# Optimization experiments

Measured on AMD Instinct MI355X. Metric: run time of the kernel, lower is better.

The kernel has to match this reference:

```python
import jax, jax.numpy as jnp
import numpy as np

B, N, T, L, H = 8, 128, 256, 32, 128


def setup_inputs() -> dict:
    key = jax.random.key(0)
    k0, k1, k2, k3, k4, k5 = jax.random.split(key, 6)
    x = jax.random.uniform(k0, (B, N, T), dtype=jnp.float32)
    s = 1.0 / np.sqrt(H)  # pytorch LSTM/Linear default init scale
    W_ih = jax.random.uniform(k1, (N, 4 * H, L), minval=-s, maxval=s, dtype=jnp.float32)
    b_ih = jax.random.uniform(k2, (N, 4 * H), minval=-s, maxval=s, dtype=jnp.float32)
    b_hh = jax.random.uniform(k3, (N, 4 * H), minval=-s, maxval=s, dtype=jnp.float32)
    W_fc = jax.random.uniform(k4, (N, N, H), minval=-s, maxval=s, dtype=jnp.float32)  # [node_i, out_j, H]
    b_fc = jax.random.uniform(k5, (N, N), minval=-s, maxval=s, dtype=jnp.float32)  # [node_i, out_j]
    return {"x": x, "W_ih": W_ih, "b_ih": b_ih, "b_hh": b_hh, "W_fc": W_fc, "b_fc": b_fc}


def reference(x, W_ih, b_ih, b_hh, W_fc, b_fc):
    # x: [B, N, T]
    Bn, Nn, Tn = x.shape
    Ln = W_ih.shape[-1]
    Hh = W_fc.shape[-1]
    Ttau = Tn - Ln  # number of prediction steps (t = L .. T-1)

    # Sliding windows x[:, i, tau:tau+L] for tau = 0..Ttau-1  -> [B, N, Ttau, L]
    idx = jnp.arange(Ttau)[:, None] + jnp.arange(Ln)[None, :]  # [Ttau, L]
    xw = x[:, :, idx]

    # Single-step LSTM with zero initial state: W_hh term vanishes.
    gates = jnp.einsum('bntl,ngl->bntg', xw, W_ih) + (b_ih + b_hh)[None, :, None, :]
    gi, gf, gg, go = jnp.split(gates, 4, axis=-1)  # pytorch order: i, f, g, o
    c = jax.nn.sigmoid(gi) * jnp.tanh(gg)          # f*c0 = 0
    h = jax.nn.sigmoid(go) * jnp.tanh(c)           # [B, N, Ttau, H]

    # Per-node fc (grouped GEMM): contributions[b, tau, j, i]
    contrib = jnp.einsum('bnth,njh->btjn', h, W_fc) + b_fc.T[None, None, :, :]

    # G[b, j, i] = mean_tau contrib[b, tau, j, i] / x[b, i, L + tau]
    denom = jnp.transpose(x[:, :, Ln:], (0, 2, 1))[:, :, None, :]  # [B, Ttau, 1, N_i]
    G = jnp.mean(contrib / denom, axis=1)                          # [B, N, N]

    X_hat = jnp.sum(contrib, axis=2) + 1e-6  # [B, Ttau, N]
    return G, X_hat
```

## Files before the change

### kernel.cpp

```cpp
#include <hip/hip_runtime.h>
#include <math.h>

#define B_  8
#define N_  128
#define T_  256
#define L_  32
#define H_  128
#define TT_ 224

typedef float f2    __attribute__((ext_vector_type(2)));
typedef float f4    __attribute__((ext_vector_type(4)));
typedef float f32x4 __attribute__((ext_vector_type(4)));
typedef short bf16x8 __attribute__((ext_vector_type(8)));

#define L2E_  1.4426950408889634f
#define L2E2_ 2.8853900817779268f

__device__ __forceinline__ unsigned pk2bf(float a, float b) {
    unsigned ua = __float_as_uint(a), ub = __float_as_uint(b);
    ua = (ua + 0x7FFFu + ((ua >> 16) & 1u)) >> 16;
    ub = (ub + 0x7FFFu + ((ub >> 16) & 1u)) >> 16;
    return ua | (ub << 16);
}
__device__ __forceinline__ float aexp2(float x) {
    float r; asm("v_exp_f32 %0, %1" : "=v"(r) : "v"(x)); return r;
}
__device__ __forceinline__ float aexp2n(float x) {
    float r; asm("v_exp_f32 %0, -%1" : "=v"(r) : "v"(x)); return r;
}
__device__ __forceinline__ float arcp(float x) {
    return __builtin_amdgcn_rcpf(x);
}

__global__ __launch_bounds__(256)
void k_pre(const float* __restrict__ W_ih, const float* __restrict__ W_fc,
           const float* __restrict__ b_ih, const float* __restrict__ b_hh,
           const float* __restrict__ b_fc,
           unsigned short* __restrict__ W3sw, float* __restrict__ wsum,
           float* __restrict__ bsum, float* __restrict__ bia_g) {
    const int n   = blockIdx.x;
    const int pid = blockIdx.y;
    const int tid = threadIdx.x;
    if (pid < 6) {
        const int idx  = pid * 256 + tid;
        const int fg   = idx >> 6;
        const int lane = idx & 63;
        const int col  = lane & 15, quad = lane >> 4;
        const int g    = fg % 3, ht = fg / 3;
        const int r    = g * 128 + ht * 16 + col;
        const int sr   = r + (r >= 128 ? 128 : 0);
        const float sc = (g == 1) ? L2E2_ : L2E_;
        const f4* src = (const f4*)(W_ih + (size_t)n * 512 * L_ + sr * L_ + quad * 8);
        f4 v0 = src[0] * sc, v1 = src[1] * sc;
        uint4 out;
        out.x = pk2bf(v0.x, v0.y); out.y = pk2bf(v0.z, v0.w);
        out.z = pk2bf(v1.x, v1.y); out.w = pk2bf(v1.z, v1.w);
        *(uint4*)&W3sw[((size_t)n * 1536 + idx) * 8] = out;
    } else {
        __shared__ f4 part[8][32];
        __shared__ float bp[2];
        {
            const int h4 = tid & 31, jg = tid >> 5;
            const f4* Wf = (const f4*)(W_fc + (size_t)n * N_ * H_) + (size_t)jg * 16 * 32 + h4;
            f4 s = {0.f, 0.f, 0.f, 0.f};
            #pragma unroll
            for (int j = 0; j < 16; ++j) s += Wf[j * 32];
            part[jg][h4] = s;
        }
        if (tid < 128) {
            float bv = b_fc[n * N_ + tid];
            #pragma unroll
            for (int off = 32; off > 0; off >>= 1) bv += __shfl_down(bv, off, 64);
            if ((tid & 63) == 0) bp[tid >> 6] = bv;
        }
        for (int i = tid; i < 384; i += 256) {
            const int sr = i + (i >= 128 ? 128 : 0);
            const float sc = (i >= 128 && i < 256) ? L2E2_ : L2E_;
            bia_g[n * 384 + i] =
                (b_ih[(size_t)n * 512 + sr] + b_hh[(size_t)n * 512 + sr]) * sc;
        }
        __syncthreads();
        if (tid < 32) {
            f4 s = part[0][tid];
            #pragma unroll
            for (int jg = 1; jg < 8; ++jg) s += part[jg][tid];
            *(f4*)&wsum[n * H_ + tid * 4] = s;
        }
        if (tid == 0) bsum[n] = bp[0] + bp[1];
    }
}

__global__ __launch_bounds__(256)
__attribute__((amdgpu_waves_per_eu(4, 4)))
void k_main(const float* __restrict__ x,
            const unsigned short* __restrict__ W3sw,
            const float* __restrict__ bia_g,
            const float* __restrict__ wsum, const float* __restrict__ bsum,
            const float* __restrict__ W_fc, const float* __restrict__ b_fc,
            float* __restrict__ G, float* __restrict__ xhat) {
    const int n   = blockIdx.x;
    const int b   = blockIdx.y;
    const int tid = threadIdx.x;
    const int w    = tid >> 6;
    const int lane = tid & 63;
    const int col  = lane & 15;
    const int quad = lane >> 4;

    __shared__ float xs[258];
    __shared__ unsigned xeo[2][128];
    __shared__ float xr[TT_];
    __shared__ uint4 xA[14 * 64];
    __shared__ float xh_part[4][TT_];
    __shared__ float hd_loc[H_];
    __shared__ float red[4];

    const uint4* wsw = (const uint4*)W3sw + (size_t)n * 24 * 64 + lane;
    union { uint4 u; bf16x8 v; } bfr[2][3];
    float biaL[2][3], wshL[2];
    #pragma unroll
    for (int ht2 = 0; ht2 < 2; ++ht2) {
        const int ht = 2 * w + ht2;
        #pragma unroll
        for (int g = 0; g < 3; ++g) {
            bfr[ht2][g].u = wsw[(size_t)(ht * 3 + g) * 64];
            biaL[ht2][g]  = bia_g[n * 384 + g * 128 + ht * 16 + col];
        }
        wshL[ht2] = wsum[n * H_ + ht * 16 + col];
    }
    const float bsum_n = bsum[n];

    xs[tid] = x[((size_t)b * N_ + n) * T_ + tid];
    if (tid < 2) xs[256 + tid] = 0.f;
    __syncthreads();
    if (tid < TT_) xr[tid] = 1.0f / xs[L_ + tid];
    if (tid < 128) {
        xeo[0][tid] = pk2bf(xs[2 * tid],     xs[2 * tid + 1]);
        xeo[1][tid] = pk2bf(xs[2 * tid + 1], xs[2 * tid + 2]);
    }
    __syncthreads();
    for (int e = tid; e < 14 * 64; e += 256) {
        const int tt = e >> 6, ln = e & 63;
        const int s  = tt * 16 + (ln & 15) + (ln >> 4) * 8;
        const int p  = s & 1, base = s >> 1;
        uint4 v;
        v.x = xeo[p][base + 0]; v.y = xeo[p][base + 1];
        v.z = xeo[p][base + 2]; v.w = xeo[p][base + 3];
        xA[e] = v;
    }
    __syncthreads();

    float hd_acc[2] = {0.f, 0.f};
    const f32x4 zero4 = {0.f, 0.f, 0.f, 0.f};

    #pragma unroll 2
    for (int ttile = 0; ttile < 14; ++ttile) {
        union { uint4 u; bf16x8 v; } af;
        af.u = xA[ttile * 64 + lane];

        const f4 xr4 = *(const f4*)&xr[ttile * 16 + quad * 4];
        float px[4];

        #pragma unroll
        for (int ht2 = 0; ht2 < 2; ++ht2) {
            f32x4 ai = __builtin_amdgcn_mfma_f32_16x16x32_bf16(af.v, bfr[ht2][0].v, zero4, 0, 0, 0);
            f32x4 ag = __builtin_amdgcn_mfma_f32_16x16x32_bf16(af.v, bfr[ht2][1].v, zero4, 0, 0, 0);
            f32x4 ao = __builtin_amdgcn_mfma_f32_16x16x32_bf16(af.v, bfr[ht2][2].v, zero4, 0, 0, 0);
            #pragma unroll
            for (int pr = 0; pr < 2; ++pr) {
                f2 gi = {ai[2*pr] + biaL[ht2][0], ai[2*pr+1] + biaL[ht2][0]};
                f2 gg = {ag[2*pr] + biaL[ht2][1], ag[2*pr+1] + biaL[ht2][1]};
                f2 go = {ao[2*pr] + biaL[ht2][2], ao[2*pr+1] + biaL[ht2][2]};
                f2 e1 = {aexp2n(gi.x), aexp2n(gi.y)};
                f2 e2 = {aexp2(gg.x),  aexp2(gg.y)};
                f2 e3 = {aexp2n(go.x), aexp2n(go.y)};
                const f2 A  = (1.f + e1) * (e2 + 1.f);
                const f2 Bv = 1.f + e3;
                const f2 AB = A * Bv;
                f2 R  = {arcp(AB.x), arcp(AB.y)};
                const f2 em = e2 - 1.f;
                const f2 t  = em * R;
                const f2 c  = t * Bv;
                const f2 c2 = c * c;
                f2 Q = c2 * -0.027698f + 0.120833f;
                Q = c2 * Q - 0.331541f;
                Q = c2 * Q + 1.0f;
                const f2 hh = t * (Q * c);
                const f2 hhv = t * Q;
                hd_acc[ht2] = fmaf(hhv.x, xr4[2*pr],   hd_acc[ht2]);
                hd_acc[ht2] = fmaf(hhv.y, xr4[2*pr+1], hd_acc[ht2]);
                px[2*pr]   = hhv.x * wshL[ht2] + (ht2 ? px[2*pr]   : 0.f);
                px[2*pr+1] = hhv.y * wshL[ht2] + (ht2 ? px[2*pr+1] : 0.f);
                (void)hh;
            }
        }
        #pragma unroll
        for (int reg = 0; reg < 4; ++reg) {
            float pv = px[reg];
            pv += __shfl_xor(pv, 1, 64);
            pv += __shfl_xor(pv, 2, 64);
            pv += __shfl_xor(pv, 4, 64);
            pv += __shfl_xor(pv, 8, 64);
            if (col == 0) xh_part[w][ttile * 16 + quad * 4 + reg] = pv;
        }
    }

    #pragma unroll
    for (int ht2 = 0; ht2 < 2; ++ht2) {
        float v = hd_acc[ht2];
        v += __shfl_xor(v, 16, 64);
        v += __shfl_xor(v, 32, 64);
        if (lane < 16) hd_loc[(2 * w + ht2) * 16 + lane] = v;
    }
    {
        float dv = (tid < TT_) ? xr[tid] : 0.f;
        #pragma unroll
        for (int off = 32; off > 0; off >>= 1) dv += __shfl_down(dv, off, 64);
        if (lane == 0) red[w] = dv;
    }
    __syncthreads();

    if (tid < TT_) {
        const float v = xh_part[0][tid] + xh_part[1][tid] +
                        xh_part[2][tid] + xh_part[3][tid];
        xhat[((size_t)b * TT_ + tid) * N_ + n] = v + bsum_n + 1e-6f;
    }

    {
        const float dinv = red[0] + red[1] + red[2] + red[3];
        const int j    = tid >> 1;
        const int half = tid & 1;
        const f4* Wf = (const f4*)(W_fc + ((size_t)n * N_ + j) * H_ + half * 64);
        float s = 0.f;
        #pragma unroll
        for (int q = 0; q < 16; ++q) {
            const f4 wv = Wf[q];
            const int hb = half * 64 + q * 4;
            s = fmaf(wv.x, hd_loc[hb + 0],
                fmaf(wv.y, hd_loc[hb + 1],
                fmaf(wv.z, hd_loc[hb + 2],
                fmaf(wv.w, hd_loc[hb + 3], s))));
        }
        s += __shfl_xor(s, 1, 64);
        if (half == 0) {
            const float bj = b_fc[n * N_ + j];
            G[(size_t)b * N_ * N_ + (size_t)j * N_ + n] =
                (s + bj * dinv) * (1.0f / 224.0f);
        }
    }
}

extern "C" void kernel_launch(void* const* d_in, const int* in_sizes, int n_in,
                              void* d_out, int out_size, void* d_ws, size_t ws_size,
                              hipStream_t stream) {
    const float* x    = (const float*)d_in[0];
    const float* W_ih = (const float*)d_in[1];
    const float* b_ih = (const float*)d_in[2];
    const float* b_hh = (const float*)d_in[3];
    const float* W_fc = (const float*)d_in[4];
    const float* b_fc = (const float*)d_in[5];

    float* G    = (float*)d_out;
    float* xhat = (float*)d_out + (size_t)B_ * N_ * N_;

    unsigned short* W3sw = (unsigned short*)d_ws;
    float* wsum   = (float*)(W3sw + (size_t)N_ * 1536 * 8);
    float* bsum   = wsum + N_ * H_;
    float* bia_g  = bsum + N_;

    k_pre<<<dim3(N_, 7), dim3(256), 0, stream>>>(W_ih, W_fc, b_ih, b_hh, b_fc,
                                                 W3sw, wsum, bsum, bia_g);
    k_main<<<dim3(N_, B_), dim3(256), 0, stream>>>(x, W3sw, bia_g, wsum, bsum,
                                                   W_fc, b_fc, G, xhat);
}
```

Before: 110.9 us.

## Split time tiles across two wave groups with 512-thread blocks in k_main

Doubles the k_main block to 512 threads. Waves are split into four hidden-tile groups and two time groups, so each wave handles 7 time tiles instead of 14. The per-time-group hidden partial sums go into a second shared buffer and are added during the W_fc dot product, which now uses four threads per output row. This cuts the serial MFMA and transcendental loop per wave to raise parallelism, at the cost of more threads per block and possible register pressure under the relaxed waves-per-EU bound.

```diff
diff --git a/kernel.cpp b/kernel.cpp
--- a/kernel.cpp
+++ b/kernel.cpp
@@ -90,18 +90,20 @@
     }
 }
 
-__global__ __launch_bounds__(256)
-__attribute__((amdgpu_waves_per_eu(4, 4)))
+__global__ __launch_bounds__(512)
+__attribute__((amdgpu_waves_per_eu(4, 8)))
 void k_main(const float* __restrict__ x,
             const unsigned short* __restrict__ W3sw,
             const float* __restrict__ bia_g,
             const float* __restrict__ wsum, const float* __restrict__ bsum,
             const float* __restrict__ W_fc, const float* __restrict__ b_fc,
             float* __restrict__ G, float* __restrict__ xhat) {
-    const int n   = blockIdx.x;
-    const int b   = blockIdx.y;
-    const int tid = threadIdx.x;
+    const int n    = blockIdx.x;
+    const int b    = blockIdx.y;
+    const int tid  = threadIdx.x;
     const int w    = tid >> 6;
+    const int hgrp = w & 3;
+    const int tgrp = w >> 2;
     const int lane = tid & 63;
     const int col  = lane & 15;
     const int quad = lane >> 4;
@@ -111,7 +113,7 @@
     __shared__ float xr[TT_];
     __shared__ uint4 xA[14 * 64];
     __shared__ float xh_part[4][TT_];
-    __shared__ float hd_loc[H_];
+    __shared__ float hd_loc2[2][H_];
     __shared__ float red[4];
 
     const uint4* wsw = (const uint4*)W3sw + (size_t)n * 24 * 64 + lane;
@@ -119,7 +121,7 @@
     float biaL[2][3], wshL[2];
     #pragma unroll
     for (int ht2 = 0; ht2 < 2; ++ht2) {
-        const int ht = 2 * w + ht2;
+        const int ht = 2 * hgrp + ht2;
         #pragma unroll
         for (int g = 0; g < 3; ++g) {
             bfr[ht2][g].u = wsw[(size_t)(ht * 3 + g) * 64];
@@ -129,8 +131,8 @@
     }
     const float bsum_n = bsum[n];
 
-    xs[tid] = x[((size_t)b * N_ + n) * T_ + tid];
-    if (tid < 2) xs[256 + tid] = 0.f;
+    if (tid < 256) xs[tid] = x[((size_t)b * N_ + n) * T_ + tid];
+    if (tid >= 256 && tid < 258) xs[tid] = 0.f;
     __syncthreads();
     if (tid < TT_) xr[tid] = 1.0f / xs[L_ + tid];
     if (tid < 128) {
@@ -138,7 +140,7 @@
         xeo[1][tid] = pk2bf(xs[2 * tid + 1], xs[2 * tid + 2]);
     }
     __syncthreads();
-    for (int e = tid; e < 14 * 64; e += 256) {
+    for (int e = tid; e < 14 * 64; e += 512) {
         const int tt = e >> 6, ln = e & 63;
         const int s  = tt * 16 + (ln & 15) + (ln >> 4) * 8;
         const int p  = s & 1, base = s >> 1;
@@ -153,7 +155,8 @@
     const f32x4 zero4 = {0.f, 0.f, 0.f, 0.f};
 
     #pragma unroll 2
-    for (int ttile = 0; ttile < 14; ++ttile) {
+    for (int tt2 = 0; tt2 < 7; ++tt2) {
+        const int ttile = tgrp * 7 + tt2;
         union { uint4 u; bf16x8 v; } af;
         af.u = xA[ttile * 64 + lane];
 
@@ -184,13 +187,11 @@
                 f2 Q = c2 * -0.027698f + 0.120833f;
                 Q = c2 * Q - 0.331541f;
                 Q = c2 * Q + 1.0f;
-                const f2 hh = t * (Q * c);
                 const f2 hhv = t * Q;
                 hd_acc[ht2] = fmaf(hhv.x, xr4[2*pr],   hd_acc[ht2]);
                 hd_acc[ht2] = fmaf(hhv.y, xr4[2*pr+1], hd_acc[ht2]);
                 px[2*pr]   = hhv.x * wshL[ht2] + (ht2 ? px[2*pr]   : 0.f);
                 px[2*pr+1] = hhv.y * wshL[ht2] + (ht2 ? px[2*pr+1] : 0.f);
-                (void)hh;
             }
         }
         #pragma unroll
@@ -200,7 +201,7 @@
             pv += __shfl_xor(pv, 2, 64);
             pv += __shfl_xor(pv, 4, 64);
             pv += __shfl_xor(pv, 8, 64);
-            if (col == 0) xh_part[w][ttile * 16 + quad * 4 + reg] = pv;
+            if (col == 0) xh_part[hgrp][ttile * 16 + quad * 4 + reg] = pv;
         }
     }
 
@@ -209,9 +210,9 @@
         float v = hd_acc[ht2];
         v += __shfl_xor(v, 16, 64);
         v += __shfl_xor(v, 32, 64);
-        if (lane < 16) hd_loc[(2 * w + ht2) * 16 + lane] = v;
-    }
-    {
+        if (lane < 16) hd_loc2[tgrp][(2 * hgrp + ht2) * 16 + lane] = v;
+    }
+    if (tid < 256) {
         float dv = (tid < TT_) ? xr[tid] : 0.f;
         #pragma unroll
         for (int off = 32; off > 0; off >>= 1) dv += __shfl_down(dv, off, 64);
@@ -227,21 +228,23 @@
 
     {
         const float dinv = red[0] + red[1] + red[2] + red[3];
-        const int j    = tid >> 1;
-        const int half = tid & 1;
-        const f4* Wf = (const f4*)(W_fc + ((size_t)n * N_ + j) * H_ + half * 64);
+        const int j   = tid >> 2;
+        const int qtr = tid & 3;
+        const f4* Wf = (const f4*)(W_fc + ((size_t)n * N_ + j) * H_ + qtr * 32);
         float s = 0.f;
         #pragma unroll
-        for (int q = 0; q < 16; ++q) {
+        for (int q = 0; q < 8; ++q) {
             const f4 wv = Wf[q];
-            const int hb = half * 64 + q * 4;
-            s = fmaf(wv.x, hd_loc[hb + 0],
-                fmaf(wv.y, hd_loc[hb + 1],
-                fmaf(wv.z, hd_loc[hb + 2],
-                fmaf(wv.w, hd_loc[hb + 3], s))));
+            const int hb = qtr * 32 + q * 4;
+            const f4 h0 = *(const f4*)&hd_loc2[0][hb];
+            const f4 h1 = *(const f4*)&hd_loc2[1][hb];
+            const f4 hv = h0 + h1;
+            s = fmaf(wv.x, hv.x, fmaf(wv.y, hv.y,
+                fmaf(wv.z, hv.z, fmaf(wv.w, hv.w, s))));
         }
         s += __shfl_xor(s, 1, 64);
-        if (half == 0) {
+        s += __shfl_xor(s, 2, 64);
+        if (qtr == 0) {
             const float bj = b_fc[n * N_ + j];
             G[(size_t)b * N_ * N_ + (size_t)j * N_ + n] =
                 (s + bj * dinv) * (1.0f / 224.0f);
@@ -269,6 +272,6 @@
 
     k_pre<<<dim3(N_, 7), dim3(256), 0, stream>>>(W_ih, W_fc, b_ih, b_hh, b_fc,
                                                  W3sw, wsum, bsum, bia_g);
-    k_main<<<dim3(N_, B_), dim3(256), 0, stream>>>(x, W3sw, bia_g, wsum, bsum,
+    k_main<<<dim3(N_, B_), dim3(512), 0, stream>>>(x, W3sw, bia_g, wsum, bsum,
                                                    W_fc, b_fc, G, xhat);
 }
```

Result: slower. 113.6 us (+2.5%).
